# Kernel optimization log

Hardware: AMD Instinct MI355X
Metric: run time of the kernel (lower is better)

Reference implementation:

```python
import jax, jax.numpy as jnp
import numpy as np

H = 64            # hidden_channels
L = 2             # num_layers
E = 300_000       # edges per relation
B = 64            # graphs in batch
NS = [100_000, 20_000, 50_000, 80_000]   # variable, value, operator, constraint
# (src_type, dst_type) for the 9 hetero relations, fixed order
RELS = [(0,1),(0,2),(0,3),(2,3),(3,3),(1,0),(2,0),(3,0),(3,2)]
R = len(RELS)
SLOPE = 0.2       # GATConv leaky_relu negative slope


def setup_inputs() -> dict:
    key = jax.random.key(0)
    ks = iter(jax.random.split(key, 64))
    inp = {}
    for n, N in zip(["x_variable", "x_value", "x_operator", "x_constraint"], NS):
        inp[n] = jax.random.normal(next(ks), (N, H), jnp.float32)
    sc = 1.0 / np.sqrt(H).astype(np.float32)
    inp["Wsrc"] = jax.random.normal(next(ks), (L, R, H, H), jnp.float32) * sc
    inp["Wdst"] = jax.random.normal(next(ks), (L, R, H, H), jnp.float32) * sc
    inp["asrc"] = jax.random.normal(next(ks), (L, R, H), jnp.float32) * sc
    inp["adst"] = jax.random.normal(next(ks), (L, R, H), jnp.float32) * sc
    inp["bias"] = jax.random.normal(next(ks), (L, R, H), jnp.float32) * 0.01
    inp["lin_w"] = jax.random.normal(next(ks), (2, 2 * H), jnp.float32) / np.sqrt(2.0 * H).astype(np.float32)
    inp["lin_b"] = jnp.zeros((2,), jnp.float32)
    for r, (s, d) in enumerate(RELS):
        inp[f"src{r}"] = jax.random.randint(next(ks), (E,), 0, NS[s], jnp.int32)
        inp[f"dst{r}"] = jax.random.randint(next(ks), (E,), 0, NS[d], jnp.int32)
    inp["batch_variable"] = jnp.sort(jax.random.randint(next(ks), (NS[0],), 0, B, jnp.int32))
    inp["batch_constraint"] = jnp.sort(jax.random.randint(next(ks), (NS[3],), 0, B, jnp.int32))
    inp["num_graphs"] = B
    return inp


def _gat(xs, xd, Ws, Wd, a_s, a_d, b, src, dst):
    """Bipartite PyG GATConv (heads=1, add_self_loops=False)."""
    hs = xs @ Ws                         # [Ns, H]
    hd = xd @ Wd                         # [Nd, H]
    al_s = hs @ a_s                      # [Ns]
    al_d = hd @ a_d                      # [Nd]
    score = jax.nn.leaky_relu(al_s[src] + al_d[dst], SLOPE)    # [E]
    nd = xd.shape[0]
    m = jax.ops.segment_max(score, dst, num_segments=nd)
    p = jnp.exp(score - m[dst])
    z = jax.ops.segment_sum(p, dst, num_segments=nd)
    alpha = p / (z[dst] + 1e-16)                               # segment softmax
    out = jax.ops.segment_sum(hs[src] * alpha[:, None], dst, num_segments=nd)
    return out + b


def _seg_mean(x, seg, n):
    s = jax.ops.segment_sum(x, seg, num_segments=n)
    c = jax.ops.segment_sum(jnp.ones((x.shape[0],), x.dtype), seg, num_segments=n)
    return s / jnp.maximum(c, 1.0)[:, None]


def reference(x_variable, x_value, x_operator, x_constraint,
              Wsrc, Wdst, asrc, adst, bias, lin_w, lin_b,
              src0, dst0, src1, dst1, src2, dst2, src3, dst3, src4, dst4,
              src5, dst5, src6, dst6, src7, dst7, src8, dst8,
              batch_variable, batch_constraint, num_graphs):
    xs = [x_variable, x_value, x_operator, x_constraint]
    srcs = [src0, src1, src2, src3, src4, src5, src6, src7, src8]
    dsts = [dst0, dst1, dst2, dst3, dst4, dst5, dst6, dst7, dst8]
    for l in range(L):
        out = [jnp.zeros((x.shape[0], H), x.dtype) for x in xs]
        for r, (s, d) in enumerate(RELS):
            out[d] = out[d] + _gat(xs[s], xs[d], Wsrc[l, r], Wdst[l, r],
                                   asrc[l, r], adst[l, r], bias[l, r],
                                   srcs[r], dsts[r])
        xs = [jax.nn.relu(o) for o in out]   # dropout is identity in eval
    vp = _seg_mean(xs[0], batch_variable, num_graphs)   # [B, H]
    cp = _seg_mean(xs[3], batch_constraint, num_graphs) # [B, H]
    return jnp.concatenate([vp, cp], axis=1) @ lin_w.T + lin_b   # [B, 2]
```

## Files before the change

kernel.cpp:

```cpp
#include <hip/hip_runtime.h>
#include <hip/hip_bf16.h>

#define NH 64
#define NRELS 9
#define NEDGE 300000
#define NGRAPH 64
#define TOTROWS 250000
#define TOTFSEG 660000
#define TOTEDGE (NRELS * NEDGE)
#define NBUCK 977
#define NBC 4
#define CHUNK 4096
#define NBLK ((TOTEDGE + CHUNK - 1) / CHUNK)
#define KCH 20
#define KSP 33
#define BKT_CAP 6144

typedef __attribute__((ext_vector_type(8))) short short8;
typedef __attribute__((ext_vector_type(4))) float f32x4;

__constant__ int c_NS[4]     = {100000, 20000, 50000, 80000};
__constant__ int c_SRC[9]    = {0,0,0,2,3,1,2,3,3};
__constant__ int c_DST[9]    = {1,2,3,3,3,0,0,0,2};
__constant__ int c_XOFF[5]   = {0,100000,120000,170000,250000};
__constant__ int c_ASOFF[10] = {0,100000,200000,300000,350000,430000,450000,500000,580000,660000};
__constant__ int c_FOFF[5]   = {0,300000,320000,420000,660000};
__constant__ int c_NRELT[4]  = {3,1,2,3};
__constant__ int c_RRANK[9]  = {0,0,0,1,2,0,1,2,1};

struct EdgePtrs { const int* s[9]; const int* d[9]; };

__device__ __forceinline__ unsigned short f2bf(float f) {
  union { __hip_bfloat16 h; unsigned short u; } c;
  c.h = __float2bfloat16(f);
  return c.u;
}

__device__ __forceinline__ float wred_max32(float v) {
#pragma unroll
  for (int o = 16; o; o >>= 1) v = fmaxf(v, __shfl_xor(v, o, 32));
  return v;
}

__global__ void k_setup(const float* Wsrc, const float* Wdst, const float* asrc,
                        const float* adst, const float* bias, float* wv, float* bsum,
                        unsigned short* wb) {
  int b = blockIdx.x, j = threadIdx.x;
  if (b < 36) {
    int r = b % 9, q = b / 9;
    int l = q >> 1, side = q & 1;
    const float* W = (side ? Wdst : Wsrc) + (l * 9 + r) * 64 * 64;
    const float* a = (side ? adst : asrc) + (l * 9 + r) * 64;
    float s = 0.f;
    for (int i = 0; i < 64; ++i) s += W[j * 64 + i] * a[i];
    wv[(side ? 1152 : 0) + (l * 9 + r) * 64 + j] = s;
  } else if (b == 36) {
    for (int l = 0; l < 2; ++l)
      for (int t = 0; t < 4; ++t) {
        float s = 0.f;
        for (int r = 0; r < 9; ++r)
          if (c_DST[r] == t) s += bias[(l * 9 + r) * 64 + j];
        bsum[(l * 4 + t) * 64 + j] = s;
      }
  } else {
    int idx = b - 37;
    int l = idx / 9, r = idx % 9;
    const float* W = Wsrc + (size_t)(l * 9 + r) * 4096;
    unsigned short* dst = wb + (size_t)(l * 9 + r) * 4096;
    for (int k = 0; k < 64; ++k)
      dst[j * 64 + k] = f2bf(W[k * 64 + j]);
  }
}

__global__ __launch_bounds__(256) void k_bhist2(EdgePtrs Eg, int* bh) {
  __shared__ int sh[NBUCK];
  for (int i = threadIdx.x; i < NBUCK; i += 256) sh[i] = 0;
  __syncthreads();
  int lo = blockIdx.x * CHUNK;
  int hi = lo + CHUNK; if (hi > TOTEDGE) hi = TOTEDGE;
  for (int gid = lo + threadIdx.x; gid < hi; gid += 256) {
    int r = gid / NEDGE, e = gid - r * NEDGE;
    int g = c_XOFF[c_DST[r]] + Eg.d[r][e];
    atomicAdd(&sh[g >> 8], 1);
  }
  __syncthreads();
  int* dst = bh + (size_t)blockIdx.x * NBUCK;
  for (int i = threadIdx.x; i < NBUCK; i += 256) dst[i] = sh[i];
}

__global__ void k_cs1(const int* bh, int* csum) {
  int blk = blockIdx.x;
  int c = blk / NBC;
  int b = (blk % NBC) * 256 + threadIdx.x;
  if (b >= NBUCK) return;
  int k0 = c * KSP;
  int k1 = k0 + KSP; if (k1 > NBLK) k1 = NBLK;
  int s = 0;
  for (int k = k0; k < k1; ++k) s += bh[(size_t)k * NBUCK + b];
  csum[(size_t)c * NBUCK + b] = s;
}

__global__ void k_cs2(int* csum, int* gbh) {
  int b = blockIdx.x * 256 + threadIdx.x;
  if (b >= NBUCK) return;
  int run = 0;
#pragma unroll
  for (int c = 0; c < KCH; ++c) {
    size_t idx = (size_t)c * NBUCK + b;
    int t = csum[idx];
    csum[idx] = run;
    run += t;
  }
  gbh[b] = run;
}

__global__ void k_cs3(int* bh, const int* csum) {
  int blk = blockIdx.x;
  int c = blk / NBC;
  int b = (blk % NBC) * 256 + threadIdx.x;
  if (b >= NBUCK) return;
  int k0 = c * KSP;
  int k1 = k0 + KSP; if (k1 > NBLK) k1 = NBLK;
  int run = csum[(size_t)c * NBUCK + b];
  for (int k = k0; k < k1; ++k) {
    size_t idx = (size_t)k * NBUCK + b;
    int t = bh[idx];
    bh[idx] = run;
    run += t;
  }
}

__global__ void k_bscan(const int* gbh, int* boff) {
  __shared__ int sd[1024];
  int t = threadIdx.x;
  int v = (t < NBUCK) ? gbh[t] : 0;
  sd[t] = v; __syncthreads();
  for (int o = 1; o < 1024; o <<= 1) {
    int x = (t >= o) ? sd[t - o] : 0; __syncthreads();
    sd[t] += x; __syncthreads();
  }
  if (t < NBUCK) boff[t] = sd[t] - v;
  if (t == 1023) boff[NBUCK] = sd[1023];
}

__global__ __launch_bounds__(256) void k_bin2(EdgePtrs Eg, const int* bh, const int* boff, int* pairs) {
  __shared__ int cur[NBUCK];
  const int* mybh = bh + (size_t)blockIdx.x * NBUCK;
  for (int i = threadIdx.x; i < NBUCK; i += 256) cur[i] = boff[i] + mybh[i];
  __syncthreads();
  int lo = blockIdx.x * CHUNK;
  int hi = lo + CHUNK; if (hi > TOTEDGE) hi = TOTEDGE;
  for (int gid = lo + threadIdx.x; gid < hi; gid += 256) {
    int r = gid / NEDGE, e = gid - r * NEDGE;
    int g = c_XOFF[c_DST[r]] + Eg.d[r][e];
    int b = g >> 8;
    int pos = atomicAdd(&cur[b], 1);
    int key = ((g & 255) << 2) | c_RRANK[r];
    pairs[pos] = (key << 20) | (c_ASOFF[r] + Eg.s[r][e]);
  }
}

__global__ __launch_bounds__(256) void k_bsort(const int* pairs, const int* boff,
                                               int* rowptr, int* asx) {
  __shared__ int spl[BKT_CAP];
  __shared__ int sout[BKT_CAP];
  __shared__ int ssc[1024];
  __shared__ int scur[1024];
  __shared__ int sws[256];
  int b = blockIdx.x, t = threadIdx.x;
  int lo = boff[b], hi = boff[b + 1];
  int n = hi - lo; if (n > BKT_CAP) n = BKT_CAP;
  for (int i = t; i < n; i += 256) spl[i] = pairs[lo + i];
  for (int i = t; i < 1024; i += 256) ssc[i] = 0;
  __syncthreads();
  for (int i = t; i < n; i += 256) atomicAdd(&ssc[((unsigned)spl[i]) >> 20], 1);
  __syncthreads();
  int c0 = ssc[t * 4], c1 = ssc[t * 4 + 1], c2 = ssc[t * 4 + 2], c3 = ssc[t * 4 + 3];
  int s = c0 + c1 + c2 + c3;
  sws[t] = s;
  __syncthreads();
  for (int o = 1; o < 256; o <<= 1) {
    int x = (t >= o) ? sws[t - o] : 0; __syncthreads();
    sws[t] += x; __syncthreads();
  }
  int base = sws[t] - s;
  ssc[t * 4]     = base;
  ssc[t * 4 + 1] = base + c0;
  ssc[t * 4 + 2] = base + c0 + c1;
  ssc[t * 4 + 3] = base + c0 + c1 + c2;
  scur[t * 4]     = ssc[t * 4];
  scur[t * 4 + 1] = ssc[t * 4 + 1];
  scur[t * 4 + 2] = ssc[t * 4 + 2];
  scur[t * 4 + 3] = ssc[t * 4 + 3];
  __syncthreads();
  int nodeBase = b << 8;
  for (int i = t; i < 1024; i += 256) {
    int l = i >> 2, rank = i & 3;
    int g = nodeBase + l;
    if (g < TOTROWS) {
      int tt = (g >= c_XOFF[1]) + (g >= c_XOFF[2]) + (g >= c_XOFF[3]);
      int nr = c_NRELT[tt];
      if (rank < nr)
        rowptr[c_FOFF[tt] + (g - c_XOFF[tt]) * nr + rank] = lo + ssc[i];
    }
  }
  if (b == 0 && t == 0) rowptr[TOTFSEG] = TOTEDGE;
  for (int i = t; i < n; i += 256) {
    int p = spl[i];
    int pos = atomicAdd(&scur[((unsigned)p) >> 20], 1);
    sout[pos] = (int)(((((unsigned)p >> 20) & 3u) << 20) | ((unsigned)p & 0xFFFFFu));
  }
  __syncthreads();
  for (int i = t; i < n; i += 256) asx[lo + i] = sout[i];
}

struct GemmAllP {
  const float* x0; const float* x1; const float* x2; const float* x3;
  const unsigned short* Wb;
  __hip_bfloat16* hs;
  float* als; float* ald;
  const float* wvs; const float* wvd;
  int act; int ntyp;
  int tbase[5];
  int typ[4];
  int nrel[4];
  int rel[4][3];
  int ndrel[4];
  int drel[4][3];
};

#define XSTR 72

__global__ __launch_bounds__(256) void k_gemma(GemmAllP G) {
  __shared__ unsigned short sx[64 * XSTR];
  __shared__ unsigned short sw[64 * XSTR];
  int bid = blockIdx.x;
  int k = 0;
#pragma unroll 3
  for (int q = 1; q < 4; ++q) if (q < G.ntyp) k += (bid >= G.tbase[q]);
  int st = G.typ[k];
  int tile = bid - G.tbase[k];
  int Ns = c_NS[st];
  const float* x = st == 0 ? G.x0 : st == 1 ? G.x1 : st == 2 ? G.x2 : G.x3;
  int base = tile * 64;
  int tid = threadIdx.x;
  for (int kk = tid; kk < 1024; kk += 256) {
    int row = kk >> 4;
    int c4 = (kk & 15) * 4;
    int gr = base + row;
    float4 v = make_float4(0.f, 0.f, 0.f, 0.f);
    if (gr < Ns) v = ((const float4*)x)[(size_t)gr * 16 + (kk & 15)];
    if (G.act) { v.x = fmaxf(v.x, 0.f); v.y = fmaxf(v.y, 0.f); v.z = fmaxf(v.z, 0.f); v.w = fmaxf(v.w, 0.f); }
    ushort4 u;
    u.x = f2bf(v.x); u.y = f2bf(v.y); u.z = f2bf(v.z); u.w = f2bf(v.w);
    *(ushort4*)&sx[row * XSTR + c4] = u;
  }
  __syncthreads();
  {
    int row = tid >> 2, part = tid & 3;
    int gr2 = base + row;
    if (gr2 < Ns) {
      float xv[16];
      const float4* xr = (const float4*)x + (size_t)gr2 * 16 + part * 4;
      float4 v0 = xr[0], v1 = xr[1], v2 = xr[2], v3 = xr[3];
      xv[0]=v0.x; xv[1]=v0.y; xv[2]=v0.z; xv[3]=v0.w;
      xv[4]=v1.x; xv[5]=v1.y; xv[6]=v1.z; xv[7]=v1.w;
      xv[8]=v2.x; xv[9]=v2.y; xv[10]=v2.z; xv[11]=v2.w;
      xv[12]=v3.x; xv[13]=v3.y; xv[14]=v3.z; xv[15]=v3.w;
      if (G.act) {
#pragma unroll
        for (int i = 0; i < 16; ++i) xv[i] = fmaxf(xv[i], 0.f);
      }
      int nrl0 = G.nrel[k];
      for (int ri = 0; ri < nrl0; ++ri) {
        int r = G.rel[k][ri];
        const float* wvp = G.wvs + r * 64 + part * 16;
        float s = 0.f;
#pragma unroll
        for (int i = 0; i < 16; ++i) s += xv[i] * wvp[i];
        s += __shfl_xor(s, 1);
        s += __shfl_xor(s, 2);
        if (part == 0) G.als[c_ASOFF[r] + gr2] = s;
      }
      int ndl = G.ndrel[k];
      for (int ri = 0; ri < ndl; ++ri) {
        int r = G.drel[k][ri];
        const float* wvp = G.wvd + r * 64 + part * 16;
        float s = 0.f;
#pragma unroll
        for (int i = 0; i < 16; ++i) s += xv[i] * wvp[i];
        s += __shfl_xor(s, 1);
        s += __shfl_xor(s, 2);
        if (part == 0)
          G.ald[c_FOFF[st] + gr2 * c_NRELT[st] + c_RRANK[r]] = s;
      }
    }
  }
  int w    = tid >> 6;
  int lane = tid & 63;
  int m    = lane & 15;
  int quad = lane >> 4;
  short8 a0 = *(const short8*)&sx[(w * 16 + m) * XSTR + quad * 8];
  short8 a1 = *(const short8*)&sx[(w * 16 + m) * XSTR + 32 + quad * 8];
  int nrl = G.nrel[k];
  for (int ri = 0; ri < nrl; ++ri) {
    int r = G.rel[k][ri];
    const unsigned short* Wb = G.Wb + (size_t)r * 4096;
    if (ri) __syncthreads();
    {
      int n = tid >> 2;
      int k0 = (tid & 3) << 4;
      short8 w0 = *(const short8*)&Wb[n * 64 + k0];
      short8 w1 = *(const short8*)&Wb[n * 64 + k0 + 8];
      *(short8*)&sw[n * XSTR + k0] = w0;
      *(short8*)&sw[n * XSTR + k0 + 8] = w1;
    }
    __syncthreads();
    f32x4 acc[4];
#pragma unroll
    for (int cb = 0; cb < 4; ++cb) acc[cb] = (f32x4)(0.f);
#pragma unroll
    for (int cb = 0; cb < 4; ++cb) {
      short8 b0 = *(const short8*)&sw[(cb * 16 + m) * XSTR + quad * 8];
      short8 b1 = *(const short8*)&sw[(cb * 16 + m) * XSTR + 32 + quad * 8];
      acc[cb] = __builtin_amdgcn_mfma_f32_16x16x32_bf16(a0, b0, acc[cb], 0, 0, 0);
      acc[cb] = __builtin_amdgcn_mfma_f32_16x16x32_bf16(a1, b1, acc[cb], 0, 0, 0);
    }
    __hip_bfloat16* hsb = G.hs + (size_t)c_ASOFF[r] * 64;
#pragma unroll
    for (int reg = 0; reg < 4; ++reg) {
      int lr = base + w * 16 + quad * 4 + reg;
      if (lr < Ns) {
#pragma unroll
        for (int cb = 0; cb < 4; ++cb)
          hsb[(size_t)lr * 64 + cb * 16 + m] = __float2bfloat16(acc[cb][reg]);
      }
    }
  }
}

struct GatherAllP {
  const __hip_bfloat16* hs;
  const float* als;
  const float* ald;
  const int* rowptr; const int* asx;
  float* xA;
  const float* bsum;
  int ntypes;
  int tbase[5];
  int typ[4];
};

__global__ __launch_bounds__(256) void k_gatherall(GatherAllP A) {
  __shared__ unsigned long long sRA[8][96];
  __shared__ float sZ[8][4];
  int bid = blockIdx.x;
  int k = 0;
#pragma unroll 3
  for (int q = 1; q < 4; ++q) if (q < A.ntypes) k += (bid >= A.tbase[q]);
  int t = A.typ[k];
  int Nd = c_NS[t];
  int lane = threadIdx.x & 63;
  int half = lane >> 5;
  int sl   = lane & 31;
  int hid  = threadIdx.x >> 5;
  int node = (bid - A.tbase[k]) * 8 + (threadIdx.x >> 6) * 2 + half;
  if (node >= Nd) return;
  int nr = c_NRELT[t];
  int fb = c_FOFF[t] + node * nr;
  int p0 = A.rowptr[fb];
  int p1 = A.rowptr[fb + nr];
  int deg = p1 - p0; if (deg > 96) deg = 96;
  float2 acc = ((const float2*)(A.bsum + t * 64))[sl];
  if (deg > 0) {
    if (sl < 4) sZ[hid][sl] = 0.f;
    const float NEG = -3.4e38f;
    const unsigned* ax = (const unsigned*)A.asx;
    unsigned rec0 = 0, rec1 = 0, rec2 = 0;
    int rk0 = 0, rk1 = 0, rk2 = 0;
    float s0 = NEG, s1 = NEG, s2 = NEG;
    if (sl < deg) {
      rec0 = ax[p0 + sl];
      rk0 = (int)((rec0 >> 20) & 3u);
      float v = A.als[rec0 & 0xFFFFFu] + A.ald[fb + rk0];
      s0 = v >= 0.f ? v : 0.2f * v;
    }
    if (sl + 32 < deg) {
      rec1 = ax[p0 + 32 + sl];
      rk1 = (int)((rec1 >> 20) & 3u);
      float v = A.als[rec1 & 0xFFFFFu] + A.ald[fb + rk1];
      s1 = v >= 0.f ? v : 0.2f * v;
    }
    if (sl + 64 < deg) {
      rec2 = ax[p0 + 64 + sl];
      rk2 = (int)((rec2 >> 20) & 3u);
      float v = A.als[rec2 & 0xFFFFFu] + A.ald[fb + rk2];
      s2 = v >= 0.f ? v : 0.2f * v;
    }
    float M = wred_max32(fmaxf(fmaxf(s0, s1), s2));
    float e0 = 0.f, e1 = 0.f, e2 = 0.f;
    if (sl < deg)      { e0 = __expf(s0 - M); atomicAdd(&sZ[hid][rk0], e0); }
    if (sl + 32 < deg) { e1 = __expf(s1 - M); atomicAdd(&sZ[hid][rk1], e1); }
    if (sl + 64 < deg) { e2 = __expf(s2 - M); atomicAdd(&sZ[hid][rk2], e2); }
    asm volatile("s_waitcnt lgkmcnt(0)" ::: "memory");
    if (sl < 3) { float z = sZ[hid][sl]; sZ[hid][sl] = 1.f / (z + 1e-16f); }
    asm volatile("s_waitcnt lgkmcnt(0)" ::: "memory");
    float a0 = e0 * sZ[hid][rk0];
    sRA[hid][sl] = ((unsigned long long)__float_as_uint(a0) << 32) | ((rec0 & 0xFFFFFu) << 7);
    if (deg > 32) {
      float a1 = e1 * sZ[hid][rk1];
      sRA[hid][32 + sl] = ((unsigned long long)__float_as_uint(a1) << 32) | ((rec1 & 0xFFFFFu) << 7);
    }
    if (deg > 64) {
      float a2 = e2 * sZ[hid][rk2];
      sRA[hid][64 + sl] = ((unsigned long long)__float_as_uint(a2) << 32) | ((rec2 & 0xFFFFFu) << 7);
    }
    const char* hsb = (const char*)A.hs;
    unsigned sl4 = (unsigned)sl * 4u;
    int nb = (deg + 7) >> 3;
    for (int g = 0; g < nb; g += 2) {
      unsigned long long raA[8], raB[8];
      unsigned hA[8], hB[8];
      bool hasB = (g + 1) < nb;
#pragma unroll
      for (int q = 0; q < 8; ++q) raA[q] = sRA[hid][g * 8 + q];
#pragma unroll
      for (int q = 0; q < 8; ++q)
        hA[q] = *(const unsigned*)(hsb + ((unsigned)(raA[q] & 0xFFFFFFFFu) + sl4));
      if (hasB) {
#pragma unroll
        for (int q = 0; q < 8; ++q) raB[q] = sRA[hid][g * 8 + 8 + q];
#pragma unroll
        for (int q = 0; q < 8; ++q)
          hB[q] = *(const unsigned*)(hsb + ((unsigned)(raB[q] & 0xFFFFFFFFu) + sl4));
      }
#pragma unroll
      for (int q = 0; q < 8; ++q) {
        float aq = __uint_as_float((unsigned)(raA[q] >> 32));
        acc.x = fmaf(aq, __uint_as_float(hA[q] << 16), acc.x);
        acc.y = fmaf(aq, __uint_as_float(hA[q] & 0xffff0000u), acc.y);
      }
      if (hasB) {
#pragma unroll
        for (int q = 0; q < 8; ++q) {
          float aq = __uint_as_float((unsigned)(raB[q] >> 32));
          acc.x = fmaf(aq, __uint_as_float(hB[q] << 16), acc.x);
          acc.y = fmaf(aq, __uint_as_float(hB[q] & 0xffff0000u), acc.y);
        }
      }
    }
  }
  float* xout = A.xA + (size_t)c_XOFF[t] * 64;
  *(float2*)&xout[(size_t)node * 64 + sl * 2] = acc;
}

__global__ void k_gbound(const int* bvar, const int* bcon, int* gs0, int* gs3) {
  int gid = blockIdx.x * 256 + threadIdx.x;
  const int N0 = 100000, N3 = 80000;
  if (gid < N0) {
    int i = gid;
    int b = bvar[i];
    int bp = i ? bvar[i - 1] : -1;
    for (int g = bp + 1; g <= b; ++g) gs0[g] = i;
    if (i == N0 - 1) for (int g = b + 1; g <= 64; ++g) gs0[g] = N0;
  } else if (gid < N0 + N3) {
    int i = gid - N0;
    int b = bcon[i];
    int bp = i ? bcon[i - 1] : -1;
    for (int g = bp + 1; g <= b; ++g) gs3[g] = i;
    if (i == N3 - 1) for (int g = b + 1; g <= 64; ++g) gs3[g] = N3;
  }
}

__global__ __launch_bounds__(256) void k_pool2(const float* xfin, const int* gs0, const int* gs3,
                                               float* partial) {
  __shared__ float4 sdv[256];
  int b = blockIdx.x;
  int sp = b >> 7;
  int rem = b & 127;
  int g = rem >> 1;
  int t = rem & 1;
  const int* gs = t ? gs3 : gs0;
  int xbase = t ? 170000 : 0;
  int lo = gs[g], hi = gs[g + 1];
  int len = hi - lo;
  int r0 = lo + (len * sp) / 8;
  int r1 = lo + (len * (sp + 1)) / 8;
  int tid = threadIdx.x;
  int rp = tid >> 4;
  int cq = tid & 15;
  float4 acc = make_float4(0.f, 0.f, 0.f, 0.f);
  for (int row = r0 + rp; row < r1; row += 16) {
    float4 v = ((const float4*)xfin)[(size_t)(xbase + row) * 16 + cq];
    acc.x += fmaxf(v.x, 0.f); acc.y += fmaxf(v.y, 0.f);
    acc.z += fmaxf(v.z, 0.f); acc.w += fmaxf(v.w, 0.f);
  }
  sdv[tid] = acc;
  __syncthreads();
  for (int o = 128; o >= 16; o >>= 1) {
    if (tid < o) {
      float4 a = sdv[tid], c = sdv[tid + o];
      a.x += c.x; a.y += c.y; a.z += c.z; a.w += c.w;
      sdv[tid] = a;
    }
    __syncthreads();
  }
  if (tid < 16) ((float4*)&partial[(size_t)b * 64])[tid] = sdv[tid];
}

__global__ void k_poolred2(const float* partial, float* pool) {
  int g = blockIdx.x >> 1;
  int t = blockIdx.x & 1;
  int col = threadIdx.x;
  float s = 0.f;
#pragma unroll
  for (int sp = 0; sp < 8; ++sp)
    s += partial[(size_t)(((sp << 7) | (g << 1) | t)) * 64 + col];
  pool[(t ? 4096 : 0) + g * 64 + col] = s;
}

__global__ void k_final(const float* pool, const int* gs0, const int* gs3,
                        const float* lin_w, const float* lin_b, float* out) {
  int k = threadIdx.x;
  int g = k >> 1, o = k & 1;
  float c0 = fmaxf((float)(gs0[g + 1] - gs0[g]), 1.f);
  float c3 = fmaxf((float)(gs3[g + 1] - gs3[g]), 1.f);
  float acc = lin_b[o];
  for (int i = 0; i < 64; ++i) {
    acc += (pool[g * 64 + i] / c0) * lin_w[o * 128 + i];
    acc += (pool[4096 + g * 64 + i] / c3) * lin_w[o * 128 + 64 + i];
  }
  out[g * 2 + o] = acc;
}

__global__ void k_bail(float* out) {
  if (threadIdx.x < 128) out[threadIdx.x] = 0.f;
}

extern "C" void kernel_launch(void* const* d_in, const int* in_sizes, int n_in,
                              void* d_out, int out_size, void* d_ws, size_t ws_size,
                              hipStream_t stream) {
  (void)in_sizes; (void)n_in; (void)out_size;
  const size_t O_XA   = 0;
  const size_t O_HS   = 16000000;
  const size_t O_ALS  = 37120000;
  const size_t O_ALD  = 37780000;
  const size_t O_WV   = 39790000;
  const size_t O_BS   = 39792304;
  const size_t O_RP   = 39792816;
  const size_t O_ASX  = 40452832;
  const size_t O_GS   = 43152832;
  const size_t O_PART = 43153088;
  const size_t O_POOL = 43218624;
  const size_t O_WB   = 43226816;
  const size_t NEED   = 43263680;

  if (ws_size < NEED * 4) {
    k_bail<<<1, 128, 0, stream>>>((float*)d_out);
    return;
  }

  const float* x0 = (const float*)d_in[0];
  const float* x1 = (const float*)d_in[1];
  const float* x2 = (const float*)d_in[2];
  const float* x3 = (const float*)d_in[3];
  const float* Wsrc = (const float*)d_in[4];
  const float* Wdst = (const float*)d_in[5];
  const float* asrc = (const float*)d_in[6];
  const float* adst = (const float*)d_in[7];
  const float* bias = (const float*)d_in[8];
  const float* lin_w = (const float*)d_in[9];
  const float* lin_b = (const float*)d_in[10];
  EdgePtrs Eg;
  for (int r = 0; r < 9; ++r) {
    Eg.s[r] = (const int*)d_in[11 + 2 * r];
    Eg.d[r] = (const int*)d_in[12 + 2 * r];
  }
  const int* bvar = (const int*)d_in[29];
  const int* bcon = (const int*)d_in[30];

  float* ws = (float*)d_ws;
  float* xA   = ws + O_XA;
  __hip_bfloat16* hs = (__hip_bfloat16*)(ws + O_HS);
  int* bh     = (int*)(ws + O_HS);
  int* pairs  = bh + (size_t)NBLK * NBUCK;
  int* gbh    = pairs + 2700000;
  int* boff   = gbh + (NBUCK + 1);
  int* csum   = boff + (NBUCK + 2);
  float* als  = ws + O_ALS;
  float* ald  = ws + O_ALD;
  float* wv   = ws + O_WV;
  float* bsum = ws + O_BS;
  int* rowptr = (int*)(ws + O_RP);
  int* asx    = (int*)(ws + O_ASX);
  int* gs0    = (int*)(ws + O_GS);
  int* gs3    = gs0 + 65;
  float* partial = ws + O_PART;
  float* pool = ws + O_POOL;
  unsigned short* wb = (unsigned short*)(ws + O_WB);

  const int h_NS[4]   = {100000, 20000, 50000, 80000};
  const int h_SRC[9]  = {0,0,0,2,3,1,2,3,3};
  const int h_DST[9]  = {1,2,3,3,3,0,0,0,2};
  const int h_XOFF[4] = {0,100000,120000,170000};

  k_setup<<<55, 64, 0, stream>>>(Wsrc, Wdst, asrc, adst, bias, wv, bsum, wb);

  k_bhist2<<<NBLK, 256, 0, stream>>>(Eg, bh);
  k_cs1<<<KCH * NBC, 256, 0, stream>>>(bh, csum);
  k_cs2<<<NBC, 256, 0, stream>>>(csum, gbh);
  k_cs3<<<KCH * NBC, 256, 0, stream>>>(bh, csum);
  k_bscan<<<1, 1024, 0, stream>>>(gbh, boff);
  k_bin2<<<NBLK, 256, 0, stream>>>(Eg, bh, boff, pairs);
  k_bsort<<<NBUCK, 256, 0, stream>>>(pairs, boff, rowptr, asx);
  k_gbound<<<(180000 + 255) / 256, 256, 0, stream>>>(bvar, bcon, gs0, gs3);

  for (int l = 0; l < 2; ++l) {
    const float* xin[4];
    if (l == 0) { xin[0] = x0; xin[1] = x1; xin[2] = x2; xin[3] = x3; }
    else {
      for (int t = 0; t < 4; ++t) xin[t] = xA + (size_t)h_XOFF[t] * 64;
    }
    int act = (l > 0);
    int relmask = l ? 0x0FC : 0x1FF;

    GemmAllP G;
    G.x0 = xin[0]; G.x1 = xin[1]; G.x2 = xin[2]; G.x3 = xin[3];
    G.Wb = wb + (size_t)l * 9 * 4096;
    G.hs = hs; G.act = act;
    G.als = als; G.ald = ald;
    G.wvs = wv + l * 576; G.wvd = wv + 1152 + l * 576;
    int ntyp = 0, cum = 0;
    for (int t = 0; t < 4; ++t) {
      int nr = 0; int rl[3]; int nd = 0; int dl[3];
      for (int r = 0; r < 9; ++r) {
        if (!((relmask >> r) & 1)) continue;
        if (h_SRC[r] == t) rl[nr++] = r;
        if (h_DST[r] == t) dl[nd++] = r;
      }
      if (!nr && !nd) continue;
      G.typ[ntyp] = t; G.nrel[ntyp] = nr; G.ndrel[ntyp] = nd;
      for (int i = 0; i < 3; ++i) {
        G.rel[ntyp][i]  = (i < nr) ? rl[i] : 0;
        G.drel[ntyp][i] = (i < nd) ? dl[i] : 0;
      }
      G.tbase[ntyp] = cum;
      cum += (h_NS[t] + 63) / 64;
      ++ntyp;
    }
    G.ntyp = ntyp; G.tbase[ntyp] = cum;
    k_gemma<<<cum, 256, 0, stream>>>(G);

    GatherAllP A;
    A.hs = hs; A.als = als; A.ald = ald;
    A.rowptr = rowptr; A.asx = asx;
    A.xA = xA;
    A.bsum = bsum + l * 256;
    int nt = 0, bcum = 0;
    for (int t = 0; t < 4; ++t) {
      if (l == 1 && (t == 1 || t == 2)) continue;
      A.typ[nt] = t;
      A.tbase[nt] = bcum;
      bcum += (h_NS[t] + 7) / 8;
      ++nt;
    }
    A.ntypes = nt; A.tbase[nt] = bcum;
    k_gatherall<<<bcum, 256, 0, stream>>>(A);
  }

  k_pool2<<<1024, 256, 0, stream>>>(xA, gs0, gs3, partial);
  k_poolred2<<<128, 64, 0, stream>>>(partial, pool);
  k_final<<<1, 128, 0, stream>>>(pool, gs0, gs3, lin_w, lin_b, (float*)d_out);
}
```

Measured before the change: 492.5 us.

## Fuse graph mean-pooling into the final-layer gather kernel via atomics

In the last layer, the gather kernel no longer writes node features to global memory. It applies relu, groups rows by graph id in shared memory, and atomically adds the partial sums into the pooling buffer, which the boundary kernel now zeroes. This removes the separate pool kernel and its full reread of the variable and constraint features. It also computes the softmax reciprocals per lane instead of in a shared-memory round trip. The cost is global atomics plus an added block-wide barrier in the gather kernel, and the pooled sum order becomes nondeterministic.

```diff
diff --git a/kernel.cpp b/kernel.cpp
--- a/kernel.cpp
+++ b/kernel.cpp
@@ -349,11 +349,16 @@
   int ntypes;
   int tbase[5];
   int typ[4];
+  int dopool;
+  const int* bvar; const int* bcon;
+  float* partial;
 };
 
 __global__ __launch_bounds__(256) void k_gatherall(GatherAllP A) {
   __shared__ unsigned long long sRA[8][96];
   __shared__ float sZ[8][4];
+  __shared__ float sPool[8][64];
+  __shared__ int sG[8];
   int bid = blockIdx.x;
   int k = 0;
 #pragma unroll 3
@@ -365,13 +370,16 @@
   int sl   = lane & 31;
   int hid  = threadIdx.x >> 5;
   int node = (bid - A.tbase[k]) * 8 + (threadIdx.x >> 6) * 2 + half;
-  if (node >= Nd) return;
+  bool active = node < Nd;
+  float2 acc = ((const float2*)(A.bsum + t * 64))[sl];
   int nr = c_NRELT[t];
   int fb = c_FOFF[t] + node * nr;
-  int p0 = A.rowptr[fb];
-  int p1 = A.rowptr[fb + nr];
-  int deg = p1 - p0; if (deg > 96) deg = 96;
-  float2 acc = ((const float2*)(A.bsum + t * 64))[sl];
+  int deg = 0, p0 = 0;
+  if (active) {
+    p0 = A.rowptr[fb];
+    int p1 = A.rowptr[fb + nr];
+    deg = p1 - p0; if (deg > 96) deg = 96;
+  }
   if (deg > 0) {
     if (sl < 4) sZ[hid][sl] = 0.f;
     const float NEG = -3.4e38f;
@@ -403,16 +411,17 @@
     if (sl + 32 < deg) { e1 = __expf(s1 - M); atomicAdd(&sZ[hid][rk1], e1); }
     if (sl + 64 < deg) { e2 = __expf(s2 - M); atomicAdd(&sZ[hid][rk2], e2); }
     asm volatile("s_waitcnt lgkmcnt(0)" ::: "memory");
-    if (sl < 3) { float z = sZ[hid][sl]; sZ[hid][sl] = 1.f / (z + 1e-16f); }
-    asm volatile("s_waitcnt lgkmcnt(0)" ::: "memory");
-    float a0 = e0 * sZ[hid][rk0];
+    float rz0 = 1.f / (sZ[hid][0] + 1e-16f);
+    float rz1 = 1.f / (sZ[hid][1] + 1e-16f);
+    float rz2 = 1.f / (sZ[hid][2] + 1e-16f);
+    float a0 = e0 * (rk0 == 0 ? rz0 : (rk0 == 1 ? rz1 : rz2));
     sRA[hid][sl] = ((unsigned long long)__float_as_uint(a0) << 32) | ((rec0 & 0xFFFFFu) << 7);
     if (deg > 32) {
-      float a1 = e1 * sZ[hid][rk1];
+      float a1 = e1 * (rk1 == 0 ? rz0 : (rk1 == 1 ? rz1 : rz2));
       sRA[hid][32 + sl] = ((unsigned long long)__float_as_uint(a1) << 32) | ((rec1 & 0xFFFFFu) << 7);
     }
     if (deg > 64) {
-      float a2 = e2 * sZ[hid][rk2];
+      float a2 = e2 * (rk2 == 0 ? rz0 : (rk2 == 1 ? rz1 : rz2));
       sRA[hid][64 + sl] = ((unsigned long long)__float_as_uint(a2) << 32) | ((rec2 & 0xFFFFFu) << 7);
     }
     const char* hsb = (const char*)A.hs;
@@ -450,11 +459,44 @@
       }
     }
   }
-  float* xout = A.xA + (size_t)c_XOFF[t] * 64;
-  *(float2*)&xout[(size_t)node * 64 + sl * 2] = acc;
-}
-
-__global__ void k_gbound(const int* bvar, const int* bcon, int* gs0, int* gs3) {
+  if (!A.dopool) {
+    if (active) {
+      float* xout = A.xA + (size_t)c_XOFF[t] * 64;
+      *(float2*)&xout[(size_t)node * 64 + sl * 2] = acc;
+    }
+    return;
+  }
+  sPool[hid][sl * 2]     = fmaxf(acc.x, 0.f);
+  sPool[hid][sl * 2 + 1] = fmaxf(acc.y, 0.f);
+  if (sl == 0) {
+    int gid = -1;
+    if (active) {
+      int g = (t == 0) ? A.bvar[node] : A.bcon[node];
+      gid = (g << 1) | (t == 3 ? 1 : 0);
+    }
+    sG[hid] = gid;
+  }
+  __syncthreads();
+  if (threadIdx.x < 64) {
+    int col = threadIdx.x;
+    int sp = (bid & 7) << 7;
+    float a = 0.f; int cg = -1;
+#pragma unroll
+    for (int i = 0; i < 8; ++i) {
+      int gi = sG[i];
+      if (gi < 0) continue;
+      float v = sPool[i][col];
+      if (gi == cg) a += v;
+      else {
+        if (cg >= 0) atomicAdd(&A.partial[(size_t)(sp | cg) * 64 + col], a);
+        cg = gi; a = v;
+      }
+    }
+    if (cg >= 0) atomicAdd(&A.partial[(size_t)(sp | cg) * 64 + col], a);
+  }
+}
+
+__global__ void k_gbound(const int* bvar, const int* bcon, int* gs0, int* gs3, float* partial) {
   int gid = blockIdx.x * 256 + threadIdx.x;
   const int N0 = 100000, N3 = 80000;
   if (gid < N0) {
@@ -469,43 +511,9 @@
     int bp = i ? bcon[i - 1] : -1;
     for (int g = bp + 1; g <= b; ++g) gs3[g] = i;
     if (i == N3 - 1) for (int g = b + 1; g <= 64; ++g) gs3[g] = N3;
-  }
-}
-
-__global__ __launch_bounds__(256) void k_pool2(const float* xfin, const int* gs0, const int* gs3,
-                                               float* partial) {
-  __shared__ float4 sdv[256];
-  int b = blockIdx.x;
-  int sp = b >> 7;
-  int rem = b & 127;
-  int g = rem >> 1;
-  int t = rem & 1;
-  const int* gs = t ? gs3 : gs0;
-  int xbase = t ? 170000 : 0;
-  int lo = gs[g], hi = gs[g + 1];
-  int len = hi - lo;
-  int r0 = lo + (len * sp) / 8;
-  int r1 = lo + (len * (sp + 1)) / 8;
-  int tid = threadIdx.x;
-  int rp = tid >> 4;
-  int cq = tid & 15;
-  float4 acc = make_float4(0.f, 0.f, 0.f, 0.f);
-  for (int row = r0 + rp; row < r1; row += 16) {
-    float4 v = ((const float4*)xfin)[(size_t)(xbase + row) * 16 + cq];
-    acc.x += fmaxf(v.x, 0.f); acc.y += fmaxf(v.y, 0.f);
-    acc.z += fmaxf(v.z, 0.f); acc.w += fmaxf(v.w, 0.f);
-  }
-  sdv[tid] = acc;
-  __syncthreads();
-  for (int o = 128; o >= 16; o >>= 1) {
-    if (tid < o) {
-      float4 a = sdv[tid], c = sdv[tid + o];
-      a.x += c.x; a.y += c.y; a.z += c.z; a.w += c.w;
-      sdv[tid] = a;
-    }
-    __syncthreads();
-  }
-  if (tid < 16) ((float4*)&partial[(size_t)b * 64])[tid] = sdv[tid];
+  } else if (gid < N0 + N3 + 65536) {
+    partial[gid - N0 - N3] = 0.f;
+  }
 }
 
 __global__ void k_poolred2(const float* partial, float* pool) {
@@ -613,7 +621,7 @@
   k_bscan<<<1, 1024, 0, stream>>>(gbh, boff);
   k_bin2<<<NBLK, 256, 0, stream>>>(Eg, bh, boff, pairs);
   k_bsort<<<NBUCK, 256, 0, stream>>>(pairs, boff, rowptr, asx);
-  k_gbound<<<(180000 + 255) / 256, 256, 0, stream>>>(bvar, bcon, gs0, gs3);
+  k_gbound<<<(180000 + 65536 + 255) / 256, 256, 0, stream>>>(bvar, bcon, gs0, gs3, partial);
 
   for (int l = 0; l < 2; ++l) {
     const float* xin[4];
@@ -656,6 +664,9 @@
     A.rowptr = rowptr; A.asx = asx;
     A.xA = xA;
     A.bsum = bsum + l * 256;
+    A.dopool = (l == 1);
+    A.bvar = bvar; A.bcon = bcon;
+    A.partial = partial;
     int nt = 0, bcum = 0;
     for (int t = 0; t < 4; ++t) {
       if (l == 1 && (t == 1 || t == 2)) continue;
@@ -668,7 +679,6 @@
     k_gatherall<<<bcum, 256, 0, stream>>>(A);
   }
 
-  k_pool2<<<1024, 256, 0, stream>>>(xA, gs0, gs3, partial);
   k_poolred2<<<128, 64, 0, stream>>>(partial, pool);
   k_final<<<1, 128, 0, stream>>>(pool, gs0, gs3, lin_w, lin_b, (float*)d_out);
 }
```

After: 487.8 us. About the same (-1.0%).
